# Performance work log

Measured on AMD Instinct MI355X. Metric: run time of the kernel, lower is better.

Reference implementation:

```python
import jax, jax.numpy as jnp
import numpy as np

HEAD_SIZE = 32


def setup_inputs() -> dict:
    key = jax.random.key(0)
    ks = jax.random.split(key, 9)
    B, N, M = 2, 512, 512
    Dq = Dk = Dv = 128
    De = 64
    H, O, OUT = 8, HEAD_SIZE, 128
    s = 0.05  # keep logits tame
    return {
        "query": jax.random.normal(ks[0], (B, N, Dq), jnp.float32),
        "key": jax.random.normal(ks[1], (B, M, Dk), jnp.float32),
        "value": jax.random.normal(ks[2], (B, M, Dv), jnp.float32),
        "edge": jax.random.normal(ks[3], (B, N, M, De), jnp.float32),
        "query_kernel": jax.random.normal(ks[4], (H, Dq, O), jnp.float32) * s,
        "key_kernel": jax.random.normal(ks[5], (H, Dk + De, O), jnp.float32) * s,
        "value_kernel": jax.random.normal(ks[6], (H, Dv, O), jnp.float32) * s,
        "projection_kernel": jax.random.normal(ks[7], (H, O, OUT), jnp.float32) * s,
        "projection_bias": jnp.zeros((OUT,), jnp.float32),
    }


def reference(query, key, value, edge, query_kernel, key_kernel,
              value_kernel, projection_kernel, projection_bias):
    # Edge-conditioned keys: concat broadcast key [B,1,M,Dk] with edge [B,N,M,De]
    B, N, _ = query.shape
    M = key.shape[-2]
    key_rep = jnp.broadcast_to(key[..., None, :, :], (B, N, M, key.shape[-1]))
    key_cat = jnp.concatenate([key_rep, edge], axis=-1)           # [B,N,M,Dk+De]
    k = jnp.einsum('bnmi,hio->bnmho', key_cat, key_kernel)        # [B,N,M,H,O]
    q = jnp.einsum('bni,hio->bnho', query, query_kernel)
    q = q / jnp.sqrt(jnp.asarray(HEAD_SIZE, q.dtype))
    v = jnp.einsum('bmi,hio->bmho', value, value_kernel)
    logits = jnp.einsum('bnho,bnmho->bhnm', q, k)                 # [B,H,N,M]
    attn = jax.nn.softmax(logits, axis=-1)
    mh = jnp.einsum('bhnm,bmho->bnho', attn, v)                   # [B,N,H,O]
    out = jnp.einsum('bnhi,hio->bno', mh, projection_kernel)
    out = out + projection_bias
    return out
```

## Files before the change

### kernel.cpp

```cpp
#include <hip/hip_runtime.h>
#include <hip/hip_bf16.h>

#define B_   2
#define N_   512
#define M_   512
#define D_   128
#define DE_  64
#define H_   8
#define O_   32
#define OUT_ 128
#define DKE_ 192
#define MP_  516

typedef unsigned short u16;
typedef unsigned int   u32;
typedef short bf16x8 __attribute__((ext_vector_type(8)));
typedef float floatx4 __attribute__((ext_vector_type(4)));

__device__ __forceinline__ u32 pk2bf(float a, float b) {
    __hip_bfloat162 h = __float22bfloat162_rn(make_float2(a, b));
    return *reinterpret_cast<u32*>(&h);
}
__device__ __forceinline__ u16 f2bf(float a) {
    __hip_bfloat16 h = __float2bfloat16(a);
    return *reinterpret_cast<u16*>(&h);
}
__device__ __forceinline__ float bf2f(u16 x) {
    return __uint_as_float(((u32)x) << 16);
}
__device__ __forceinline__ bf16x8 cvt8(const float4 a, const float4 b) {
    union { u32 u[4]; bf16x8 v; } r;
    r.u[0] = pk2bf(a.x, a.y); r.u[1] = pk2bf(a.z, a.w);
    r.u[2] = pk2bf(b.x, b.y); r.u[3] = pk2bf(b.z, b.w);
    return r.v;
}

__global__ __launch_bounds__(256) void k_proj(
    const float* __restrict__ query, const float* __restrict__ Wq,
    const float* __restrict__ Wk,
    const float* __restrict__ value, const float* __restrict__ Wv,
    const float* __restrict__ key,
    u16* __restrict__ qE, u16* __restrict__ vP, u16* __restrict__ keyF)
{
    const int t = threadIdx.x;
    __shared__ float Xs[8][D_];
    __shared__ float qh[8][H_ * O_];

    if (blockIdx.x < 128) {
        const int r0 = blockIdx.x * 8;
        reinterpret_cast<float4*>(&Xs[0][0])[t] =
            reinterpret_cast<const float4*>(query + (size_t)r0 * D_)[t];
        __syncthreads();
        {
            float acc[8] = {0,0,0,0,0,0,0,0};
            const float* wcol = Wq + (t >> 5) * (D_ * O_) + (t & 31);
            for (int k = 0; k < D_; k += 4) {
                const float w0 = wcol[(k+0) * O_];
                const float w1 = wcol[(k+1) * O_];
                const float w2 = wcol[(k+2) * O_];
                const float w3 = wcol[(k+3) * O_];
#pragma unroll
                for (int r = 0; r < 8; ++r) {
                    const float4 x = *reinterpret_cast<const float4*>(&Xs[r][k]);
                    acc[r] += x.x * w0 + x.y * w1 + x.z * w2 + x.w * w3;
                }
            }
#pragma unroll
            for (int r = 0; r < 8; ++r) qh[r][t] = acc[r] * 0.17677669529663687f;
        }
        __syncthreads();

        for (int s = 0; s < 6; ++s) {
            const int hj = t + 256 * s;
            const int h  = hj / DKE_;
            float w[O_];
#pragma unroll
            for (int i = 0; i < O_ / 4; ++i) {
                const float4 x = reinterpret_cast<const float4*>(Wk + (size_t)hj * O_)[i];
                w[4*i] = x.x; w[4*i+1] = x.y; w[4*i+2] = x.z; w[4*i+3] = x.w;
            }
#pragma unroll
            for (int r = 0; r < 8; ++r) {
                const float* qrow = &qh[r][h * O_];
                float a = 0.f;
#pragma unroll
                for (int i = 0; i < O_ / 4; ++i) {
                    const float4 qx = *reinterpret_cast<const float4*>(qrow + 4*i);
                    a += qx.x * w[4*i] + qx.y * w[4*i+1] + qx.z * w[4*i+2] + qx.w * w[4*i+3];
                }
                qE[(size_t)(r0 + r) * (H_ * DKE_) + hj] = f2bf(a);
            }
        }
    } else if (blockIdx.x < 256) {
        const int r0 = (blockIdx.x - 128) * 8;
        reinterpret_cast<float4*>(&Xs[0][0])[t] =
            reinterpret_cast<const float4*>(value + (size_t)r0 * D_)[t];
        __syncthreads();

        float acc[8] = {0,0,0,0,0,0,0,0};
        const float* wcol = Wv + (t >> 5) * (D_ * O_) + (t & 31);
        for (int k = 0; k < D_; k += 4) {
            const float w0 = wcol[(k+0) * O_];
            const float w1 = wcol[(k+1) * O_];
            const float w2 = wcol[(k+2) * O_];
            const float w3 = wcol[(k+3) * O_];
#pragma unroll
            for (int r = 0; r < 8; ++r) {
                const float4 x = *reinterpret_cast<const float4*>(&Xs[r][k]);
                acc[r] += x.x * w0 + x.y * w1 + x.z * w2 + x.w * w3;
            }
        }
        const int bb = r0 >> 9, m0 = r0 & 511;
        union { u32 u[4]; uint4 q; } pk;
        pk.u[0] = pk2bf(acc[0], acc[1]);
        pk.u[1] = pk2bf(acc[2], acc[3]);
        pk.u[2] = pk2bf(acc[4], acc[5]);
        pk.u[3] = pk2bf(acc[6], acc[7]);
        *reinterpret_cast<uint4*>(
            vP + ((((size_t)bb * 64) + (m0 >> 3)) * 256 + t) * 8) = pk.q;
    } else {
        const int kb = blockIdx.x - 256;
        const int bb = kb >> 5, tl = kb & 31;
        const int kk = t >> 6, l = t & 63;
        const int br = l & 15, q = l >> 4;
        const float* src = key + ((size_t)bb * M_ + tl * 16 + br) * D_ + kk * 32 + q * 8;
        const float4 f0 = *reinterpret_cast<const float4*>(src);
        const float4 f1 = *reinterpret_cast<const float4*>(src + 4);
        union { bf16x8 v; uint4 u; } r;
        r.v = cvt8(f0, f1);
        *reinterpret_cast<uint4*>(
            keyF + ((((size_t)bb * 32 + tl) * 4 + kk) * 64 + l) * 8) = r.u;
    }
}

__global__ __launch_bounds__(256, 4) void k_attn(
    const float* __restrict__ edge,
    const u16* __restrict__ qE, const u16* __restrict__ vP,
    const u16* __restrict__ keyF,
    const float* __restrict__ Wp, const float* __restrict__ bias,
    float* __restrict__ out)
{
    const int idx  = blockIdx.x;
    const int b    = idx >> 9;
    const int t    = threadIdx.x;
    const int lane = t & 63;
    const int wv   = t >> 6;

    __shared__ __attribute__((aligned(16))) float attn_s[H_][MP_];
    __shared__ __attribute__((aligned(16))) u16 elds[4][2][2][64][8];
    __shared__ float mh_s[H_ * O_];
    __shared__ float part_s[2][OUT_];

    const int br = lane & 15;
    const int q  = lane >> 4;

    bf16x8 afr[6];
    if (br < 8) {
        const u16* ab = qE + (size_t)idx * (H_ * DKE_) + br * DKE_;
#pragma unroll
        for (int kk = 0; kk < 6; ++kk)
            afr[kk] = *reinterpret_cast<const bf16x8*>(ab + kk * 32 + q * 8);
    } else {
#pragma unroll
        for (int kk = 0; kk < 6; ++kk) afr[kk] = bf16x8{0,0,0,0,0,0,0,0};
    }

    const float* eb  = edge + (size_t)idx * (M_ * DE_);
    const u16*   kfb = keyF + (size_t)b * (32 * 4 * 64 * 8);

    float4 ef[4];
    {
        const float* tb = eb + (size_t)wv * 1024;
#pragma unroll
        for (int i = 0; i < 4; ++i)
            ef[i] = reinterpret_cast<const float4*>(tb)[i * 64 + lane];
    }
    for (int it = 0; it < 8; ++it) {
        const int tl  = it * 4 + wv;
        const int buf = it & 1;
#pragma unroll
        for (int i = 0; i < 4; ++i) {
            const int c    = i * 64 + lane;
            const int row  = c >> 4, col4 = c & 15;
            uint2 p;
            p.x = pk2bf(ef[i].x, ef[i].y);
            p.y = pk2bf(ef[i].z, ef[i].w);
            *reinterpret_cast<uint2*>(
                &elds[wv][buf][col4 >> 3][(((col4 >> 1) & 3) << 4) + row][(col4 & 1) * 4]) = p;
        }
        if (it < 7) {
            const float* tb = eb + (size_t)(tl + 4) * 1024;
#pragma unroll
            for (int i = 0; i < 4; ++i)
                ef[i] = reinterpret_cast<const float4*>(tb)[i * 64 + lane];
        }
        floatx4 acc = {0.f, 0.f, 0.f, 0.f};
        const u16* kf = kfb + (size_t)tl * 4 * 512 + lane * 8;
#pragma unroll
        for (int kk = 0; kk < 4; ++kk) {
            const bf16x8 bfr = *reinterpret_cast<const bf16x8*>(kf + kk * 512);
            acc = __builtin_amdgcn_mfma_f32_16x16x32_bf16(afr[kk], bfr, acc, 0, 0, 0);
        }
#pragma unroll
        for (int kk = 0; kk < 2; ++kk) {
            const bf16x8 bfr = *reinterpret_cast<const bf16x8*>(&elds[wv][buf][kk][lane][0]);
            acc = __builtin_amdgcn_mfma_f32_16x16x32_bf16(afr[4 + kk], bfr, acc, 0, 0, 0);
        }
        if (q < 2) {
#pragma unroll
            for (int i = 0; i < 4; ++i)
                attn_s[q * 4 + i][tl * 16 + br] = acc[i];
        }
    }
    __syncthreads();

    {
        const int h = t >> 5, ml = t & 31;
        float mx = -3.4e38f;
#pragma unroll 2
        for (int j = 0; j < 16; ++j) mx = fmaxf(mx, attn_s[h][ml + 32 * j]);
#pragma unroll
        for (int mask = 16; mask >= 1; mask >>= 1) mx = fmaxf(mx, __shfl_xor(mx, mask, 64));
        float sum = 0.f;
#pragma unroll 2
        for (int j = 0; j < 16; ++j) {
            const int m = ml + 32 * j;
            const float p = __expf(attn_s[h][m] - mx);
            attn_s[h][m] = p;
            sum += p;
        }
#pragma unroll
        for (int mask = 16; mask >= 1; mask >>= 1) sum += __shfl_xor(sum, mask, 64);
        const float inv = 1.f / sum;
#pragma unroll 2
        for (int j = 0; j < 16; ++j) attn_s[h][ml + 32 * j] *= inv;
    }
    __syncthreads();

    {
        const int hh = t >> 5;
        const u16* vb = vP + (size_t)b * (64 * 256 * 8);
        float a0 = 0.f, a1 = 0.f;
        for (int m0 = 0; m0 < M_; m0 += 8) {
            const bf16x8 v8 = *reinterpret_cast<const bf16x8*>(
                vb + ((size_t)(m0 >> 3) * 256 + t) * 8);
            const float4 w0 = *reinterpret_cast<const float4*>(&attn_s[hh][m0]);
            const float4 w1 = *reinterpret_cast<const float4*>(&attn_s[hh][m0 + 4]);
            a0 += w0.x * bf2f((u16)v8[0]) + w0.y * bf2f((u16)v8[1])
                + w0.z * bf2f((u16)v8[2]) + w0.w * bf2f((u16)v8[3]);
            a1 += w1.x * bf2f((u16)v8[4]) + w1.y * bf2f((u16)v8[5])
                + w1.z * bf2f((u16)v8[6]) + w1.w * bf2f((u16)v8[7]);
        }
        mh_s[t] = a0 + a1;
    }
    __syncthreads();

    {
        const int half = t >> 7;
        const int c = t & 127;
        float acc = 0.f;
        const int j0 = half * 128;
#pragma unroll 8
        for (int jj = 0; jj < 128; ++jj)
            acc += mh_s[j0 + jj] * Wp[(size_t)(j0 + jj) * OUT_ + c];
        part_s[half][c] = acc;
    }
    __syncthreads();
    if (t < OUT_)
        out[(size_t)idx * OUT_ + t] = part_s[0][t] + part_s[1][t] + bias[t];
}

extern "C" void kernel_launch(void* const* d_in, const int* in_sizes, int n_in,
                              void* d_out, int out_size, void* d_ws, size_t ws_size,
                              hipStream_t stream)
{
    const float* query = (const float*)d_in[0];
    const float* key   = (const float*)d_in[1];
    const float* value = (const float*)d_in[2];
    const float* edge  = (const float*)d_in[3];
    const float* Wq    = (const float*)d_in[4];
    const float* Wk    = (const float*)d_in[5];
    const float* Wv    = (const float*)d_in[6];
    const float* Wp    = (const float*)d_in[7];
    const float* bias  = (const float*)d_in[8];
    float* out = (float*)d_out;

    u16* qE_ws = (u16*)d_ws;
    u16* vP_ws = qE_ws + (size_t)B_ * N_ * H_ * DKE_;
    u16* kF_ws = vP_ws + (size_t)B_ * 64 * 256 * 8;

    k_proj<<<320,  256, 0, stream>>>(query, Wq, Wk, value, Wv, key, qE_ws, vP_ws, kF_ws);
    k_attn<<<1024, 256, 0, stream>>>(edge, qE_ws, vP_ws, kF_ws, Wp, bias, out);
}
```

Baseline: 241.0 us.

## Fuse query projection into attention kernel and process two query rows per block

Moves the query and key-kernel projection (qE) out of the projection kernel and computes it inside the attention kernel in shared memory, removing the qE workspace round trip. Each 512-thread block now handles two query rows, filling all 16 MFMA rows (8 heads x 2 rows) instead of 8, so key-fragment and value loads are shared across both rows. Edge tiles in LDS get an XOR swizzle to reduce bank conflicts. In exchange, Wq and Wk projection work is now redone per block, and the larger blocks with more shared memory may lower occupancy.

New measurement: 259.3 us. 7.6% more time.

```diff
diff --git a/kernel.cpp b/kernel.cpp
--- a/kernel.cpp
+++ b/kernel.cpp
@@ -36,63 +36,15 @@
 }
 
 __global__ __launch_bounds__(256) void k_proj(
-    const float* __restrict__ query, const float* __restrict__ Wq,
-    const float* __restrict__ Wk,
     const float* __restrict__ value, const float* __restrict__ Wv,
     const float* __restrict__ key,
-    u16* __restrict__ qE, u16* __restrict__ vP, u16* __restrict__ keyF)
+    u16* __restrict__ vP, u16* __restrict__ keyF)
 {
     const int t = threadIdx.x;
     __shared__ float Xs[8][D_];
-    __shared__ float qh[8][H_ * O_];
 
     if (blockIdx.x < 128) {
         const int r0 = blockIdx.x * 8;
-        reinterpret_cast<float4*>(&Xs[0][0])[t] =
-            reinterpret_cast<const float4*>(query + (size_t)r0 * D_)[t];
-        __syncthreads();
-        {
-            float acc[8] = {0,0,0,0,0,0,0,0};
-            const float* wcol = Wq + (t >> 5) * (D_ * O_) + (t & 31);
-            for (int k = 0; k < D_; k += 4) {
-                const float w0 = wcol[(k+0) * O_];
-                const float w1 = wcol[(k+1) * O_];
-                const float w2 = wcol[(k+2) * O_];
-                const float w3 = wcol[(k+3) * O_];
-#pragma unroll
-                for (int r = 0; r < 8; ++r) {
-                    const float4 x = *reinterpret_cast<const float4*>(&Xs[r][k]);
-                    acc[r] += x.x * w0 + x.y * w1 + x.z * w2 + x.w * w3;
-                }
-            }
-#pragma unroll
-            for (int r = 0; r < 8; ++r) qh[r][t] = acc[r] * 0.17677669529663687f;
-        }
-        __syncthreads();
-
-        for (int s = 0; s < 6; ++s) {
-            const int hj = t + 256 * s;
-            const int h  = hj / DKE_;
-            float w[O_];
-#pragma unroll
-            for (int i = 0; i < O_ / 4; ++i) {
-                const float4 x = reinterpret_cast<const float4*>(Wk + (size_t)hj * O_)[i];
-                w[4*i] = x.x; w[4*i+1] = x.y; w[4*i+2] = x.z; w[4*i+3] = x.w;
-            }
-#pragma unroll
-            for (int r = 0; r < 8; ++r) {
-                const float* qrow = &qh[r][h * O_];
-                float a = 0.f;
-#pragma unroll
-                for (int i = 0; i < O_ / 4; ++i) {
-                    const float4 qx = *reinterpret_cast<const float4*>(qrow + 4*i);
-                    a += qx.x * w[4*i] + qx.y * w[4*i+1] + qx.z * w[4*i+2] + qx.w * w[4*i+3];
-                }
-                qE[(size_t)(r0 + r) * (H_ * DKE_) + hj] = f2bf(a);
-            }
-        }
-    } else if (blockIdx.x < 256) {
-        const int r0 = (blockIdx.x - 128) * 8;
         reinterpret_cast<float4*>(&Xs[0][0])[t] =
             reinterpret_cast<const float4*>(value + (size_t)r0 * D_)[t];
         __syncthreads();
@@ -119,7 +71,7 @@
         *reinterpret_cast<uint4*>(
             vP + ((((size_t)bb * 64) + (m0 >> 3)) * 256 + t) * 8) = pk.q;
     } else {
-        const int kb = blockIdx.x - 256;
+        const int kb = blockIdx.x - 128;
         const int bb = kb >> 5, tl = kb & 31;
         const int kk = t >> 6, l = t & 63;
         const int br = l & 15, q = l >> 4;
@@ -133,141 +85,225 @@
     }
 }
 
-__global__ __launch_bounds__(256, 4) void k_attn(
+__global__ __launch_bounds__(512, 4) void k_attn(
+    const float* __restrict__ query, const float* __restrict__ Wq,
+    const float* __restrict__ Wk,
     const float* __restrict__ edge,
-    const u16* __restrict__ qE, const u16* __restrict__ vP,
-    const u16* __restrict__ keyF,
+    const u16* __restrict__ vP, const u16* __restrict__ keyF,
     const float* __restrict__ Wp, const float* __restrict__ bias,
     float* __restrict__ out)
 {
-    const int idx  = blockIdx.x;
-    const int b    = idx >> 9;
+    const int pr   = blockIdx.x;
+    const int idx0 = pr * 2;
+    const int b    = pr >> 8;
     const int t    = threadIdx.x;
     const int lane = t & 63;
     const int wv   = t >> 6;
 
-    __shared__ __attribute__((aligned(16))) float attn_s[H_][MP_];
-    __shared__ __attribute__((aligned(16))) u16 elds[4][2][2][64][8];
-    __shared__ float mh_s[H_ * O_];
-    __shared__ float part_s[2][OUT_];
+    __shared__ __attribute__((aligned(16))) float attn_s[2][H_][MP_];
+    __shared__ __attribute__((aligned(16))) u16 elds[8][2][2048];
+    __shared__ float mh_s[2][2][256];
+    __shared__ float part_s[2][2][OUT_];
+
+    float* Xq   = &attn_s[0][0][0];
+    float* qh_s = Xq + 256;
+    u16*  qE_l  = (u16*)(qh_s + 512);
+
+    const float* eb0 = edge + (size_t)idx0 * (M_ * DE_);
+    const float* eb1 = eb0 + (M_ * DE_);
+    float4 ef0[4], ef1[4];
+    {
+        const float* tb0 = eb0 + (size_t)wv * 1024;
+        const float* tb1 = eb1 + (size_t)wv * 1024;
+#pragma unroll
+        for (int i = 0; i < 4; ++i) {
+            ef0[i] = reinterpret_cast<const float4*>(tb0)[i * 64 + lane];
+            ef1[i] = reinterpret_cast<const float4*>(tb1)[i * 64 + lane];
+        }
+    }
+
+    if (t < 64)
+        reinterpret_cast<float4*>(Xq)[t] =
+            reinterpret_cast<const float4*>(query + (size_t)idx0 * D_)[t];
+    __syncthreads();
+    {
+        const int n = t >> 8, col = t & 255;
+        const float* wcol = Wq + (col >> 5) * (D_ * O_) + (col & 31);
+        const float* x = Xq + n * D_;
+        float acc = 0.f;
+        for (int k = 0; k < D_; k += 4) {
+            const float4 xv = *reinterpret_cast<const float4*>(x + k);
+            acc += xv.x * wcol[(k+0) * O_] + xv.y * wcol[(k+1) * O_]
+                 + xv.z * wcol[(k+2) * O_] + xv.w * wcol[(k+3) * O_];
+        }
+        qh_s[n * 256 + col] = acc * 0.17677669529663687f;
+    }
+    __syncthreads();
+#pragma unroll
+    for (int s = 0; s < 3; ++s) {
+        const int hj = t + 512 * s;
+        const int h  = hj / DKE_;
+        float w[O_];
+#pragma unroll
+        for (int i = 0; i < O_ / 4; ++i) {
+            const float4 x = reinterpret_cast<const float4*>(Wk + (size_t)hj * O_)[i];
+            w[4*i] = x.x; w[4*i+1] = x.y; w[4*i+2] = x.z; w[4*i+3] = x.w;
+        }
+#pragma unroll
+        for (int n = 0; n < 2; ++n) {
+            const float* qrow = qh_s + n * 256 + h * O_;
+            float a = 0.f;
+#pragma unroll
+            for (int i = 0; i < O_ / 4; ++i) {
+                const float4 qx = *reinterpret_cast<const float4*>(qrow + 4*i);
+                a += qx.x * w[4*i] + qx.y * w[4*i+1] + qx.z * w[4*i+2] + qx.w * w[4*i+3];
+            }
+            qE_l[n * 1536 + hj] = f2bf(a);
+        }
+    }
+    __syncthreads();
 
     const int br = lane & 15;
     const int q  = lane >> 4;
-
-    bf16x8 afr[6];
-    if (br < 8) {
-        const u16* ab = qE + (size_t)idx * (H_ * DKE_) + br * DKE_;
-#pragma unroll
-        for (int kk = 0; kk < 6; ++kk)
-            afr[kk] = *reinterpret_cast<const bf16x8*>(ab + kk * 32 + q * 8);
-    } else {
-#pragma unroll
-        for (int kk = 0; kk < 6; ++kk) afr[kk] = bf16x8{0,0,0,0,0,0,0,0};
-    }
-
-    const float* eb  = edge + (size_t)idx * (M_ * DE_);
-    const u16*   kfb = keyF + (size_t)b * (32 * 4 * 64 * 8);
-
-    float4 ef[4];
-    {
-        const float* tb = eb + (size_t)wv * 1024;
-#pragma unroll
-        for (int i = 0; i < 4; ++i)
-            ef[i] = reinterpret_cast<const float4*>(tb)[i * 64 + lane];
-    }
-    for (int it = 0; it < 8; ++it) {
-        const int tl  = it * 4 + wv;
-        const int buf = it & 1;
+    const int nsel = br >> 3, hsel = br & 7;
+    bf16x8 afr_k[4], afr_e0[2], afr_e1[2];
+    {
+        const u16* ab = qE_l + nsel * 1536 + hsel * DKE_;
+#pragma unroll
+        for (int kk = 0; kk < 4; ++kk)
+            afr_k[kk] = *reinterpret_cast<const bf16x8*>(ab + kk * 32 + q * 8);
+        const bf16x8 ze = {0,0,0,0,0,0,0,0};
+#pragma unroll
+        for (int kk = 0; kk < 2; ++kk) {
+            const bf16x8 fr = *reinterpret_cast<const bf16x8*>(ab + 128 + kk * 32 + q * 8);
+            afr_e0[kk] = nsel ? ze : fr;
+            afr_e1[kk] = nsel ? fr : ze;
+        }
+    }
+    __syncthreads();
+
+    const u16* kfb = keyF + (size_t)b * (32 * 4 * 64 * 8);
+
+    for (int it = 0; it < 4; ++it) {
+        const int tl = it * 8 + wv;
 #pragma unroll
         for (int i = 0; i < 4; ++i) {
-            const int c    = i * 64 + lane;
-            const int row  = c >> 4, col4 = c & 15;
-            uint2 p;
-            p.x = pk2bf(ef[i].x, ef[i].y);
-            p.y = pk2bf(ef[i].z, ef[i].w);
-            *reinterpret_cast<uint2*>(
-                &elds[wv][buf][col4 >> 3][(((col4 >> 1) & 3) << 4) + row][(col4 & 1) * 4]) = p;
-        }
-        if (it < 7) {
-            const float* tb = eb + (size_t)(tl + 4) * 1024;
-#pragma unroll
-            for (int i = 0; i < 4; ++i)
-                ef[i] = reinterpret_cast<const float4*>(tb)[i * 64 + lane];
+            const int c = i * 64 + lane;
+            const int row = c >> 4, col4 = c & 15;
+            const int kk = col4 >> 3, y = (col4 >> 1) & 3;
+            const int g = (kk * 64 + y * 16 + row) ^ (y << 1);
+            const int off = g * 8 + (col4 & 1) * 4;
+            uint2 p0, p1;
+            p0.x = pk2bf(ef0[i].x, ef0[i].y); p0.y = pk2bf(ef0[i].z, ef0[i].w);
+            p1.x = pk2bf(ef1[i].x, ef1[i].y); p1.y = pk2bf(ef1[i].z, ef1[i].w);
+            *reinterpret_cast<uint2*>(&elds[wv][0][off]) = p0;
+            *reinterpret_cast<uint2*>(&elds[wv][1][off]) = p1;
+        }
+        if (it < 3) {
+            const float* tb0 = eb0 + (size_t)(tl + 8) * 1024;
+            const float* tb1 = eb1 + (size_t)(tl + 8) * 1024;
+#pragma unroll
+            for (int i = 0; i < 4; ++i) {
+                ef0[i] = reinterpret_cast<const float4*>(tb0)[i * 64 + lane];
+                ef1[i] = reinterpret_cast<const float4*>(tb1)[i * 64 + lane];
+            }
         }
         floatx4 acc = {0.f, 0.f, 0.f, 0.f};
-        const u16* kf = kfb + (size_t)tl * 4 * 512 + lane * 8;
+        const u16* kf = kfb + (size_t)tl * 2048 + lane * 8;
 #pragma unroll
         for (int kk = 0; kk < 4; ++kk) {
             const bf16x8 bfr = *reinterpret_cast<const bf16x8*>(kf + kk * 512);
-            acc = __builtin_amdgcn_mfma_f32_16x16x32_bf16(afr[kk], bfr, acc, 0, 0, 0);
-        }
+            acc = __builtin_amdgcn_mfma_f32_16x16x32_bf16(afr_k[kk], bfr, acc, 0, 0, 0);
+        }
+        const int swz = ((lane >> 4) & 3) << 1;
 #pragma unroll
         for (int kk = 0; kk < 2; ++kk) {
-            const bf16x8 bfr = *reinterpret_cast<const bf16x8*>(&elds[wv][buf][kk][lane][0]);
-            acc = __builtin_amdgcn_mfma_f32_16x16x32_bf16(afr[4 + kk], bfr, acc, 0, 0, 0);
-        }
-        if (q < 2) {
-#pragma unroll
-            for (int i = 0; i < 4; ++i)
-                attn_s[q * 4 + i][tl * 16 + br] = acc[i];
-        }
-    }
-    __syncthreads();
-
-    {
-        const int h = t >> 5, ml = t & 31;
+            const int g = (kk * 64 + lane) ^ swz;
+            const bf16x8 b0 = *reinterpret_cast<const bf16x8*>(&elds[wv][0][g * 8]);
+            acc = __builtin_amdgcn_mfma_f32_16x16x32_bf16(afr_e0[kk], b0, acc, 0, 0, 0);
+        }
+#pragma unroll
+        for (int kk = 0; kk < 2; ++kk) {
+            const int g = (kk * 64 + lane) ^ swz;
+            const bf16x8 b1 = *reinterpret_cast<const bf16x8*>(&elds[wv][1][g * 8]);
+            acc = __builtin_amdgcn_mfma_f32_16x16x32_bf16(afr_e1[kk], b1, acc, 0, 0, 0);
+        }
+#pragma unroll
+        for (int i = 0; i < 4; ++i) {
+            const int rr = q * 4 + i;
+            attn_s[rr >> 3][rr & 7][tl * 16 + br] = acc[i];
+        }
+    }
+    __syncthreads();
+
+    {
+        const int r = t >> 5, ml = t & 31;
+        const int n = r >> 3, h = r & 7;
         float mx = -3.4e38f;
 #pragma unroll 2
-        for (int j = 0; j < 16; ++j) mx = fmaxf(mx, attn_s[h][ml + 32 * j]);
+        for (int j = 0; j < 16; ++j) mx = fmaxf(mx, attn_s[n][h][ml + 32 * j]);
 #pragma unroll
         for (int mask = 16; mask >= 1; mask >>= 1) mx = fmaxf(mx, __shfl_xor(mx, mask, 64));
         float sum = 0.f;
 #pragma unroll 2
         for (int j = 0; j < 16; ++j) {
             const int m = ml + 32 * j;
-            const float p = __expf(attn_s[h][m] - mx);
-            attn_s[h][m] = p;
+            const float p = __expf(attn_s[n][h][m] - mx);
+            attn_s[n][h][m] = p;
             sum += p;
         }
 #pragma unroll
         for (int mask = 16; mask >= 1; mask >>= 1) sum += __shfl_xor(sum, mask, 64);
         const float inv = 1.f / sum;
 #pragma unroll 2
-        for (int j = 0; j < 16; ++j) attn_s[h][ml + 32 * j] *= inv;
-    }
-    __syncthreads();
-
-    {
-        const int hh = t >> 5;
-        const u16* vb = vP + (size_t)b * (64 * 256 * 8);
-        float a0 = 0.f, a1 = 0.f;
-        for (int m0 = 0; m0 < M_; m0 += 8) {
-            const bf16x8 v8 = *reinterpret_cast<const bf16x8*>(
-                vb + ((size_t)(m0 >> 3) * 256 + t) * 8);
-            const float4 w0 = *reinterpret_cast<const float4*>(&attn_s[hh][m0]);
-            const float4 w1 = *reinterpret_cast<const float4*>(&attn_s[hh][m0 + 4]);
-            a0 += w0.x * bf2f((u16)v8[0]) + w0.y * bf2f((u16)v8[1])
-                + w0.z * bf2f((u16)v8[2]) + w0.w * bf2f((u16)v8[3]);
-            a1 += w1.x * bf2f((u16)v8[4]) + w1.y * bf2f((u16)v8[5])
-                + w1.z * bf2f((u16)v8[6]) + w1.w * bf2f((u16)v8[7]);
-        }
-        mh_s[t] = a0 + a1;
-    }
-    __syncthreads();
-
-    {
-        const int half = t >> 7;
-        const int c = t & 127;
+        for (int j = 0; j < 16; ++j) attn_s[n][h][ml + 32 * j] *= inv;
+    }
+    __syncthreads();
+
+    {
+        const int tt = t & 255, half = t >> 8, hh = tt >> 5;
+        const u16* vb = vP + (size_t)b * (64 * 256 * 8)
+                      + ((size_t)(half * 32) * 256 + tt) * 8;
+        const int mbase = half * 256;
+        float a00 = 0.f, a01 = 0.f, a10 = 0.f, a11 = 0.f;
+#pragma unroll 4
+        for (int j = 0; j < 32; ++j) {
+            const bf16x8 v8 = *reinterpret_cast<const bf16x8*>(vb + (size_t)j * 2048);
+            const int m0 = mbase + j * 8;
+            const float4 w00 = *reinterpret_cast<const float4*>(&attn_s[0][hh][m0]);
+            const float4 w01 = *reinterpret_cast<const float4*>(&attn_s[0][hh][m0 + 4]);
+            const float4 w10 = *reinterpret_cast<const float4*>(&attn_s[1][hh][m0]);
+            const float4 w11 = *reinterpret_cast<const float4*>(&attn_s[1][hh][m0 + 4]);
+            const float v0 = bf2f((u16)v8[0]), v1 = bf2f((u16)v8[1]);
+            const float v2 = bf2f((u16)v8[2]), v3 = bf2f((u16)v8[3]);
+            const float v4 = bf2f((u16)v8[4]), v5 = bf2f((u16)v8[5]);
+            const float v6 = bf2f((u16)v8[6]), v7 = bf2f((u16)v8[7]);
+            a00 += w00.x * v0 + w00.y * v1 + w00.z * v2 + w00.w * v3;
+            a01 += w01.x * v4 + w01.y * v5 + w01.z * v6 + w01.w * v7;
+            a10 += w10.x * v0 + w10.y * v1 + w10.z * v2 + w10.w * v3;
+            a11 += w11.x * v4 + w11.y * v5 + w11.z * v6 + w11.w * v7;
+        }
+        mh_s[0][half][tt] = a00 + a01;
+        mh_s[1][half][tt] = a10 + a11;
+    }
+    __syncthreads();
+
+    {
+        const int n = t >> 8, hseg = (t >> 7) & 1, c = t & 127;
+        const int j0 = hseg * 128;
         float acc = 0.f;
-        const int j0 = half * 128;
 #pragma unroll 8
-        for (int jj = 0; jj < 128; ++jj)
-            acc += mh_s[j0 + jj] * Wp[(size_t)(j0 + jj) * OUT_ + c];
-        part_s[half][c] = acc;
-    }
-    __syncthreads();
-    if (t < OUT_)
-        out[(size_t)idx * OUT_ + t] = part_s[0][t] + part_s[1][t] + bias[t];
+        for (int jj = 0; jj < 128; ++jj) {
+            const int j = j0 + jj;
+            acc += (mh_s[n][0][j] + mh_s[n][1][j]) * Wp[(size_t)j * OUT_ + c];
+        }
+        part_s[n][hseg][c] = acc;
+    }
+    __syncthreads();
+    if (t < 256) {
+        const int n = t >> 7, c = t & 127;
+        out[(size_t)(idx0 + n) * OUT_ + c] = part_s[n][0][c] + part_s[n][1][c] + bias[c];
+    }
 }
 
 extern "C" void kernel_launch(void* const* d_in, const int* in_sizes, int n_in,
@@ -285,10 +321,9 @@
     const float* bias  = (const float*)d_in[8];
     float* out = (float*)d_out;
 
-    u16* qE_ws = (u16*)d_ws;
-    u16* vP_ws = qE_ws + (size_t)B_ * N_ * H_ * DKE_;
+    u16* vP_ws = (u16*)d_ws;
     u16* kF_ws = vP_ws + (size_t)B_ * 64 * 256 * 8;
 
-    k_proj<<<320,  256, 0, stream>>>(query, Wq, Wk, value, Wv, key, qE_ws, vP_ws, kF_ws);
-    k_attn<<<1024, 256, 0, stream>>>(edge, qE_ws, vP_ws, kF_ws, Wp, bias, out);
-}
+    k_proj<<<192, 256, 0, stream>>>(value, Wv, key, vP_ws, kF_ws);
+    k_attn<<<512, 512, 0, stream>>>(query, Wq, Wk, edge, vP_ws, kF_ws, Wp, bias, out);
+}
```

## Remap edge loads to match MFMA layout, single-buffer LDS, raise occupancy, unroll PV loop

Applied to the files above, without the earlier changes.

Each lane now loads the edge elements in an order matching the MFMA B-fragment layout, so the bf16 values are written to LDS contiguously instead of through a scattered index. This removes the double buffer and halves the edge LDS footprint. Launch bounds rise from 4 to 6 blocks per CU, and the attention-times-V loop is unrolled with cheaper bf16 unpacking using shifts and masks. The new global access pattern is less coalesced per instruction, and the single buffer could race across iterations if waves are not implicitly synchronised.

After: 249.9 us. 3.7% more time.

```diff
diff --git a/kernel.cpp b/kernel.cpp
--- a/kernel.cpp
+++ b/kernel.cpp
@@ -24,9 +24,6 @@
 __device__ __forceinline__ u16 f2bf(float a) {
     __hip_bfloat16 h = __float2bfloat16(a);
     return *reinterpret_cast<u16*>(&h);
-}
-__device__ __forceinline__ float bf2f(u16 x) {
-    return __uint_as_float(((u32)x) << 16);
 }
 __device__ __forceinline__ bf16x8 cvt8(const float4 a, const float4 b) {
     union { u32 u[4]; bf16x8 v; } r;
@@ -133,7 +130,7 @@
     }
 }
 
-__global__ __launch_bounds__(256, 4) void k_attn(
+__global__ __launch_bounds__(256, 6) void k_attn(
     const float* __restrict__ edge,
     const u16* __restrict__ qE, const u16* __restrict__ vP,
     const u16* __restrict__ keyF,
@@ -147,12 +144,20 @@
     const int wv   = t >> 6;
 
     __shared__ __attribute__((aligned(16))) float attn_s[H_][MP_];
-    __shared__ __attribute__((aligned(16))) u16 elds[4][2][2][64][8];
+    __shared__ __attribute__((aligned(16))) u16 elds[4][1024];
     __shared__ float mh_s[H_ * O_];
     __shared__ float part_s[2][OUT_];
 
     const int br = lane & 15;
     const int q  = lane >> 4;
+
+    const int base16 = ((lane >> 1) & 15) * 16 + ((lane >> 5) << 1) + (lane & 1);
+
+    const float4* tb = reinterpret_cast<const float4*>(edge + (size_t)idx * (M_ * DE_));
+    float4 ef[4];
+#pragma unroll
+    for (int i = 0; i < 4; ++i)
+        ef[i] = tb[wv * 256 + base16 + i * 4];
 
     bf16x8 afr[6];
     if (br < 8) {
@@ -165,37 +170,23 @@
         for (int kk = 0; kk < 6; ++kk) afr[kk] = bf16x8{0,0,0,0,0,0,0,0};
     }
 
-    const float* eb  = edge + (size_t)idx * (M_ * DE_);
-    const u16*   kfb = keyF + (size_t)b * (32 * 4 * 64 * 8);
-
-    float4 ef[4];
-    {
-        const float* tb = eb + (size_t)wv * 1024;
-#pragma unroll
-        for (int i = 0; i < 4; ++i)
-            ef[i] = reinterpret_cast<const float4*>(tb)[i * 64 + lane];
-    }
+    const u16* kfb = keyF + (size_t)b * (32 * 4 * 64 * 8);
+
     for (int it = 0; it < 8; ++it) {
-        const int tl  = it * 4 + wv;
-        const int buf = it & 1;
+        const int tl = it * 4 + wv;
 #pragma unroll
         for (int i = 0; i < 4; ++i) {
-            const int c    = i * 64 + lane;
-            const int row  = c >> 4, col4 = c & 15;
             uint2 p;
-            p.x = pk2bf(ef[i].x, ef[i].y);
-            p.y = pk2bf(ef[i].z, ef[i].w);
-            *reinterpret_cast<uint2*>(
-                &elds[wv][buf][col4 >> 3][(((col4 >> 1) & 3) << 4) + row][(col4 & 1) * 4]) = p;
+            p.x = pk2bf(ef[i].x, ef[i].y); p.y = pk2bf(ef[i].z, ef[i].w);
+            *reinterpret_cast<uint2*>(&elds[wv][i * 256 + lane * 4]) = p;
         }
         if (it < 7) {
-            const float* tb = eb + (size_t)(tl + 4) * 1024;
 #pragma unroll
             for (int i = 0; i < 4; ++i)
-                ef[i] = reinterpret_cast<const float4*>(tb)[i * 64 + lane];
+                ef[i] = tb[(tl + 4) * 256 + base16 + i * 4];
         }
         floatx4 acc = {0.f, 0.f, 0.f, 0.f};
-        const u16* kf = kfb + (size_t)tl * 4 * 512 + lane * 8;
+        const u16* kf = kfb + (size_t)tl * 2048 + lane * 8;
 #pragma unroll
         for (int kk = 0; kk < 4; ++kk) {
             const bf16x8 bfr = *reinterpret_cast<const bf16x8*>(kf + kk * 512);
@@ -203,7 +194,7 @@
         }
 #pragma unroll
         for (int kk = 0; kk < 2; ++kk) {
-            const bf16x8 bfr = *reinterpret_cast<const bf16x8*>(&elds[wv][buf][kk][lane][0]);
+            const bf16x8 bfr = *reinterpret_cast<const bf16x8*>(&elds[wv][(kk * 64 + lane) * 8]);
             acc = __builtin_amdgcn_mfma_f32_16x16x32_bf16(afr[4 + kk], bfr, acc, 0, 0, 0);
         }
         if (q < 2) {
@@ -239,17 +230,23 @@
 
     {
         const int hh = t >> 5;
-        const u16* vb = vP + (size_t)b * (64 * 256 * 8);
+        const u16* vb = vP + (size_t)b * (64 * 256 * 8) + (size_t)t * 8;
         float a0 = 0.f, a1 = 0.f;
-        for (int m0 = 0; m0 < M_; m0 += 8) {
-            const bf16x8 v8 = *reinterpret_cast<const bf16x8*>(
-                vb + ((size_t)(m0 >> 3) * 256 + t) * 8);
-            const float4 w0 = *reinterpret_cast<const float4*>(&attn_s[hh][m0]);
-            const float4 w1 = *reinterpret_cast<const float4*>(&attn_s[hh][m0 + 4]);
-            a0 += w0.x * bf2f((u16)v8[0]) + w0.y * bf2f((u16)v8[1])
-                + w0.z * bf2f((u16)v8[2]) + w0.w * bf2f((u16)v8[3]);
-            a1 += w1.x * bf2f((u16)v8[4]) + w1.y * bf2f((u16)v8[5])
-                + w1.z * bf2f((u16)v8[6]) + w1.w * bf2f((u16)v8[7]);
+#pragma unroll 8
+        for (int j = 0; j < 64; ++j) {
+            const uint4 v4 = *reinterpret_cast<const uint4*>(vb + (size_t)j * 2048);
+            const float4 w0 = *reinterpret_cast<const float4*>(&attn_s[hh][j * 8]);
+            const float4 w1 = *reinterpret_cast<const float4*>(&attn_s[hh][j * 8 + 4]);
+            const float v0 = __uint_as_float(v4.x << 16);
+            const float v1 = __uint_as_float(v4.x & 0xffff0000u);
+            const float v2 = __uint_as_float(v4.y << 16);
+            const float v3 = __uint_as_float(v4.y & 0xffff0000u);
+            const float v4f = __uint_as_float(v4.z << 16);
+            const float v5 = __uint_as_float(v4.z & 0xffff0000u);
+            const float v6 = __uint_as_float(v4.w << 16);
+            const float v7 = __uint_as_float(v4.w & 0xffff0000u);
+            a0 += w0.x * v0 + w0.y * v1 + w0.z * v2 + w0.w * v3;
+            a1 += w1.x * v4f + w1.y * v5 + w1.z * v6 + w1.w * v7;
         }
         mh_s[t] = a0 + a1;
     }
```
